# Optimization experiments

Measured on AMD Instinct MI355X. Metric: run time of the kernel, lower is better.

The kernel has to match this reference:

```python
import jax, jax.numpy as jnp
import numpy as np
import math

B, SEQ, H, HKV, D = 2, 2048, 32, 8, 128
BLOCK, LOCAL_BLOCKS, VERT_STRIDE = 64, 16, 8
NB = SEQ // BLOCK


def _build_layout():
    # local + vertical-strided causal block-sparse layout (homo heads),
    # converted from CSR to a padded [NB, max_nnz] column-index table.
    q_idx = np.arange(NB)[:, None]
    k_idx = np.arange(NB)[None, :]
    dense = (k_idx <= q_idx) & ((q_idx - k_idx < LOCAL_BLOCKS) | ((k_idx + 1) % VERT_STRIDE == 0))
    max_nnz = int(dense.sum(1).max())  # == 18 for NB=32, local=16, stride=8
    cols = np.zeros((NB, max_nnz), np.int32)
    valid = np.zeros((NB, max_nnz), np.bool_)
    for i in range(NB):
        c = np.nonzero(dense[i])[0]
        cols[i, :c.size] = c
        valid[i, :c.size] = True
    return jnp.asarray(cols), jnp.asarray(valid)


def setup_inputs() -> dict:
    key = jax.random.key(0)
    kq, kk, kv = jax.random.split(key, 3)
    q = jax.random.normal(kq, (B, SEQ, H, D), jnp.float32)
    k = jax.random.normal(kk, (B, SEQ, HKV, D), jnp.float32)
    v = jax.random.normal(kv, (B, SEQ, HKV, D), jnp.float32)
    layout_cols, layout_mask = _build_layout()
    return {"q": q, "k": k, "v": v, "layout_cols": layout_cols, "layout_mask": layout_mask}


def _attn(q, k, v, layout_cols, layout_mask):
    Bn, S, Hq, Dh = q.shape
    Hkv = k.shape[2]
    g = Hq // Hkv               # GQA group size (q_k_ratio)
    nb, nnz = layout_cols.shape
    blk = S // nb               # block_size
    sm_scale = 1.0 / math.sqrt(Dh)
    # reshape to blocks; keep KV at Hkv heads (no repeat) and group q heads
    qb = q.reshape(Bn, nb, blk, Hkv, g, Dh).transpose(0, 3, 4, 1, 2, 5)  # [B,Hkv,g,nb,blk,D]
    kb = k.reshape(Bn, nb, blk, Hkv, Dh).transpose(0, 3, 1, 2, 4)        # [B,Hkv,nb,blk,D]
    vb = v.reshape(Bn, nb, blk, Hkv, Dh).transpose(0, 3, 1, 2, 4)
    # gather only the attended K/V blocks per query block (honors block sparsity)
    kg = jnp.take(kb, layout_cols, axis=2)  # [B,Hkv,nb,nnz,blk,D]
    vg = jnp.take(vb, layout_cols, axis=2)
    scores = jnp.einsum('bhgqmd,bhqknd->bhgqmkn', qb, kg) * sm_scale  # [B,Hkv,g,nb,blk,nnz,blk]
    # token-level causal mask + padded-column mask (past_len = 0 for prefill)
    q_tok = jnp.arange(nb)[:, None] * blk + jnp.arange(blk)[None, :]            # [nb,blk]
    k_tok = layout_cols[:, :, None] * blk + jnp.arange(blk)[None, None, :]      # [nb,nnz,blk]
    valid = layout_mask[:, None, :, None] & (k_tok[:, None] <= q_tok[:, :, None, None])  # [nb,blk,nnz,blk]
    scores = jnp.where(valid[None, None, None], scores, -jnp.inf)
    p = jax.nn.softmax(scores.reshape(Bn, Hkv, g, nb, blk, nnz * blk), axis=-1).reshape(scores.shape)
    out = jnp.einsum('bhgqmkn,bhqknd->bhgqmd', p, vg)
    return out.transpose(0, 3, 4, 1, 2, 5).reshape(Bn, S, Hq, Dh)


def reference(q, k, v, layout_cols, layout_mask):
    return _attn(q, k, v, layout_cols, layout_mask)
```

## Files before the change

### kernel.cpp

```cpp
#include <hip/hip_runtime.h>

#define B_    2
#define SEQ_  2048
#define H_    32
#define HKV_  8
#define D_    128
#define BLK_  64
#define NB_   32
#define LOCAL_ 16
#define VERT_  8

#define PSTR 72
#define NTASK 512
#define NBLOCK 512

typedef __attribute__((ext_vector_type(8))) short bf16x8;
typedef __attribute__((ext_vector_type(4))) float f32x4;
typedef __attribute__((ext_vector_type(16))) float f32x16;

__device__ __forceinline__ unsigned short f2bf(float f) {
    union { float f; unsigned u; } x; x.f = f;
    unsigned u = x.u;
    return (unsigned short)((u + 0x7FFFu + ((u >> 16) & 1u)) >> 16);
}

__device__ __forceinline__ unsigned pk2(float a, float b) {
#if defined(__has_builtin) && __has_builtin(__builtin_amdgcn_cvt_pk_bf16_f32)
    typedef __attribute__((ext_vector_type(2))) __bf16 bf2;
    bf2 r = __builtin_amdgcn_cvt_pk_bf16_f32(a, b);
    unsigned u; __builtin_memcpy(&u, &r, 4); return u;
#else
    return (unsigned)f2bf(a) | ((unsigned)f2bf(b) << 16);
#endif
}

__device__ __forceinline__ void pswap(unsigned &a, unsigned &b) {
#if defined(__has_builtin) && __has_builtin(__builtin_amdgcn_permlane32_swap)
    auto r = __builtin_amdgcn_permlane32_swap((int)a, (int)b, false, false);
    a = (unsigned)r[0]; b = (unsigned)r[1];
#else
    asm("v_permlane32_swap_b32 %0, %1" : "+v"(a), "+v"(b));
#endif
}

__device__ __forceinline__ f32x16 zero16() {
    f32x16 z;
#pragma unroll
    for (int i = 0; i < 16; ++i) z[i] = 0.f;
    return z;
}

__device__ __forceinline__ int next_valid(int qb, int j) {
    for (++j; j <= qb; ++j)
        if (((qb - j) < LOCAL_) || (((j + 1) & (VERT_ - 1)) == 0)) return j;
    return qb + 1;
}

__device__ __forceinline__ void dma16(const unsigned short* g, unsigned short* l) {
    __builtin_amdgcn_global_load_lds(
        (const __attribute__((address_space(1))) unsigned int*)g,
        (__attribute__((address_space(3))) unsigned int*)l, 16, 0, 0);
}

__global__ __launch_bounds__(256)
void prepass_kernel(const float* __restrict__ kg, const float* __restrict__ vg,
                    unsigned short* __restrict__ Kws, unsigned short* __restrict__ Vws) {
    __shared__ unsigned short Vt[D_ * 72];
    const int bid = blockIdx.x;
    const int b   = bid >> 8;
    const int hkv = (bid >> 5) & 7;
    const int jb  = bid & 31;
    const int tid = threadIdx.x;
    const int rs  = HKV_ * D_;

    const float* kbase = kg + ((size_t)(b * SEQ_ + jb * BLK_) * HKV_ + hkv) * D_;
    const float* vbase = vg + ((size_t)(b * SEQ_ + jb * BLK_) * HKV_ + hkv) * D_;
    unsigned short* Kdst = Kws + ((size_t)(b * 8 + hkv) * SEQ_ + jb * BLK_) * D_;
    unsigned short* Vdst = Vws + ((size_t)(b * 8 + hkv) * NB_ + jb) * (D_ * BLK_);

#pragma unroll
    for (int t = 0; t < 4; ++t) {
        const int q = t * 256 + tid;
        const int row = q >> 4, c = q & 15;
        const float* p = kbase + (size_t)row * rs + c * 8;
        const float4 a = *(const float4*)p;
        const float4 d4 = *(const float4*)(p + 4);
        uint4 u = { pk2(a.x, a.y), pk2(a.z, a.w), pk2(d4.x, d4.y), pk2(d4.z, d4.w) };
        *(uint4*)&Kdst[row * 128 + ((c ^ (row & 15)) << 3)] = u;
    }
#pragma unroll
    for (int t = 0; t < 8; ++t) {
        const int q = t * 256 + tid;
        const int pos = q >> 5, c4 = q & 31;
        const float4 v4 = *(const float4*)(vbase + (size_t)pos * rs + c4 * 4);
        const unsigned u0 = pk2(v4.x, v4.y), u1 = pk2(v4.z, v4.w);
        Vt[(c4 * 4 + 0) * 72 + pos] = (unsigned short)u0;
        Vt[(c4 * 4 + 1) * 72 + pos] = (unsigned short)(u0 >> 16);
        Vt[(c4 * 4 + 2) * 72 + pos] = (unsigned short)u1;
        Vt[(c4 * 4 + 3) * 72 + pos] = (unsigned short)(u1 >> 16);
    }
    __syncthreads();
#pragma unroll
    for (int t = 0; t < 4; ++t) {
        const int q = t * 256 + tid;
        const int d = q >> 3, c = q & 7;
        const uint2 q0 = *(const uint2*)&Vt[d * 72 + c * 8];
        const uint2 q1 = *(const uint2*)&Vt[d * 72 + c * 8 + 4];
        uint4 u = { q0.x, q0.y, q1.x, q1.y };
        *(uint4*)&Vdst[d * 64 + ((c ^ (d & 7)) << 3)] = u;
    }
}

__global__ __launch_bounds__(512, 2)
void sparse_attn_v5(const float* __restrict__ qg, float* __restrict__ outg,
                    const unsigned short* __restrict__ Kws,
                    const unsigned short* __restrict__ Vws,
                    unsigned* __restrict__ ctr) {
    __shared__ __align__(16) unsigned short Kb[2][BLK_ * D_];
    __shared__ __align__(16) unsigned short Vb[2][D_ * BLK_];
    __shared__ unsigned taskLds;

    const int tid  = threadIdx.x;
    const int wave = tid >> 6;
    const int lane = tid & 63;
    const int q5   = lane & 31;
    const int h    = lane >> 5;
    const int hsub = wave >> 1;
    const int rt2  = wave & 1;

    int cskA[8];
#pragma unroll
    for (int dk = 0; dk < 8; ++dk) cskA[dk] = ((((dk * 2) | h) ^ (lane & 15)) << 3);
    int csvB[4];
#pragma unroll
    for (int kc = 0; kc < 4; ++kc) csvB[kc] = ((((kc * 2) | h) ^ (lane & 7)) << 3);

    const float c2 = 0.12751649736230723f;
    const short oneb = (short)0x3F80;
    const bf16x8 ones = {oneb, oneb, oneb, oneb, oneb, oneb, oneb, oneb};

    for (;;) {
        __syncthreads();
        if (tid == 0) taskLds = atomicAdd(ctr, 1u);
        __syncthreads();
        const unsigned t = taskLds;
        if (t >= NTASK) break;

        const int qb  = 31 - (int)(t >> 4);
        const int bh  = (int)(t & 15);
        const int b   = bh >> 3;
        const int hkv = bh & 7;
        const int head = hkv * 4 + hsub;

        const unsigned short* Kbh = Kws + (size_t)(b * 8 + hkv) * SEQ_ * D_;
        const unsigned short* Vbh = Vws + (size_t)(b * 8 + hkv) * NB_ * (D_ * BLK_);

        int j = next_valid(qb, -1);
        {
            const size_t off = (size_t)j * (BLK_ * D_);
#pragma unroll
            for (int i = 0; i < 2; ++i) {
                dma16(Kbh + off + i * 4096 + tid * 8, &Kb[0][i * 4096 + wave * 512]);
                dma16(Vbh + off + i * 4096 + tid * 8, &Vb[0][i * 4096 + wave * 512]);
            }
        }

        bf16x8 qf[8];
        {
            const int row = qb * BLK_ + rt2 * 32 + q5;
            const float* qp = qg + ((size_t)(b * SEQ_ + row) * H_ + head) * D_ + h * 8;
#pragma unroll
            for (int dk = 0; dk < 8; ++dk) {
                const float4 a = *(const float4*)(qp + dk * 16);
                const float4 c = *(const float4*)(qp + dk * 16 + 4);
                uint4 u = { pk2(a.x, a.y), pk2(a.z, a.w), pk2(c.x, c.y), pk2(c.z, c.w) };
                __builtin_memcpy(&qf[dk], &u, 16);
            }
        }

        f32x16 lacc = zero16();
        f32x16 o_acc[4];
#pragma unroll
        for (int dt = 0; dt < 4; ++dt) o_acc[dt] = zero16();

        __syncthreads();
        int it = 0;
        while (j <= qb) {
            const int jn = next_valid(qb, j);
            const int cur = it & 1;
            if (jn <= qb) {
                const size_t off = (size_t)jn * (BLK_ * D_);
#pragma unroll
                for (int i = 0; i < 2; ++i) {
                    dma16(Kbh + off + i * 4096 + tid * 8, &Kb[cur ^ 1][i * 4096 + wave * 512]);
                    dma16(Vbh + off + i * 4096 + tid * 8, &Vb[cur ^ 1][i * 4096 + wave * 512]);
                }
            }

            const bool diag  = (j == qb);
            const bool diagw = diag && (rt2 == 0);

            const unsigned short* kb = Kb[cur];
            f32x16 s0 = zero16(), s1 = zero16();
            {
                const unsigned short* k0r = kb + q5 * 128;
                const unsigned short* k1r = kb + (32 + q5) * 128;
#pragma unroll
                for (int dk = 0; dk < 8; ++dk) {
                    const bf16x8 kf0 = *(const bf16x8*)(k0r + cskA[dk]);
                    s0 = __builtin_amdgcn_mfma_f32_32x32x16_bf16(kf0, qf[dk], s0, 0, 0, 0);
                }
                if (!diagw) {
#pragma unroll
                    for (int dk = 0; dk < 8; ++dk) {
                        const bf16x8 kf1 = *(const bf16x8*)(k1r + cskA[dk]);
                        s1 = __builtin_amdgcn_mfma_f32_32x32x16_bf16(kf1, qf[dk], s1, 0, 0, 0);
                    }
                }
            }

            if (diag) {
                if (rt2 == 0) {
#pragma unroll
                    for (int r = 0; r < 16; ++r) {
                        const int crow = (r & 3) + 8 * (r >> 2) + 4 * h;
                        if (crow > q5) s0[r] = -INFINITY;
                    }
                } else {
#pragma unroll
                    for (int r = 0; r < 16; ++r) {
                        const int crow = (r & 3) + 8 * (r >> 2) + 4 * h;
                        if (crow > q5) s1[r] = -INFINITY;
                    }
                }
            }

#pragma unroll
            for (int r = 0; r < 16; ++r) s0[r] = exp2f(s0[r] * c2);
            if (!diagw) {
#pragma unroll
                for (int r = 0; r < 16; ++r) s1[r] = exp2f(s1[r] * c2);
            }

            bf16x8 pa[4];
#pragma unroll
            for (int kc = 0; kc < 4; ++kc) {
                if (kc >= 2 && diagw) continue;
                const f32x16 &pp = (kc >= 2) ? s1 : s0;
                const int b0 = (kc & 1) * 8;
                unsigned A0 = pk2(pp[b0 + 0], pp[b0 + 1]);
                unsigned B0 = pk2(pp[b0 + 4], pp[b0 + 5]);
                unsigned A1 = pk2(pp[b0 + 2], pp[b0 + 3]);
                unsigned B1 = pk2(pp[b0 + 6], pp[b0 + 7]);
                pswap(A0, B0);
                pswap(A1, B1);
                uint4 u = { A0, A1, B0, B1 };
                __builtin_memcpy(&pa[kc], &u, 16);
                lacc = __builtin_amdgcn_mfma_f32_32x32x16_bf16(pa[kc], ones, lacc, 0, 0, 0);
            }

            const unsigned short* vb = Vb[cur];
#pragma unroll
            for (int dt = 0; dt < 4; ++dt) {
                const unsigned short* vrow = vb + (dt * 32 + q5) * 64;
#pragma unroll
                for (int kc = 0; kc < 4; ++kc) {
                    if (kc >= 2 && diagw) continue;
                    const bf16x8 vf = *(const bf16x8*)(vrow + csvB[kc]);
                    o_acc[dt] = __builtin_amdgcn_mfma_f32_32x32x16_bf16(pa[kc], vf, o_acc[dt], 0, 0, 0);
                }
            }

            __syncthreads();
            j = jn; ++it;
        }

        const int rowbase = qb * BLK_ + rt2 * 32;
#pragma unroll
        for (int r = 0; r < 16; ++r) {
            const int row = rowbase + (r & 3) + 8 * (r >> 2) + 4 * h;
            const float inv = 1.0f / lacc[r];
            float* op = outg + ((size_t)(b * SEQ_ + row) * H_ + head) * D_ + q5;
            op[0]  = o_acc[0][r] * inv;
            op[32] = o_acc[1][r] * inv;
            op[64] = o_acc[2][r] * inv;
            op[96] = o_acc[3][r] * inv;
        }
    }
}

#define KSTR 136
#define VSTR 72
__global__ __launch_bounds__(1024)
void sparse_attn_v1(const float* __restrict__ qg, const float* __restrict__ kg,
                    const float* __restrict__ vg, float* __restrict__ outg,
                    unsigned* __restrict__ ctr) {
    __shared__ __align__(16) unsigned short Klds[BLK_ * KSTR];
    __shared__ __align__(16) unsigned short Vlds[D_ * VSTR];
    __shared__ __align__(16) unsigned short Plds[16 * 16 * PSTR];
    __shared__ unsigned taskLds;

    const int tid  = threadIdx.x;
    const int wave = tid >> 6;
    const int lane = tid & 63;
    const int l15  = lane & 15;
    const int quad = lane >> 4;
    const int hsub = wave >> 2;
    const int rt   = wave & 3;

    const int srow0 = tid >> 5, srow1 = srow0 + 32;
    const int sc4   = tid & 31;
    const int kld0  = srow0 * KSTR + sc4 * 4, kld1 = srow1 * KSTR + sc4 * 4;
    const int vd    = sc4 * 4;
    const int vskew = (sc4 & 7) << 3;
    const int vp0   = (srow0 + vskew) & 63, vp1 = (srow1 + vskew) & 63;
    const size_t stoff0 = (size_t)srow0 * (HKV_ * D_) + sc4 * 4;
    const size_t stoff1 = (size_t)srow1 * (HKV_ * D_) + sc4 * 4;

    const float c2 = 0.12751649736230723f;
    const short oneb = (short)0x3F80;
    const bf16x8 ones = {oneb, oneb, oneb, oneb, oneb, oneb, oneb, oneb};
    unsigned short* pl = &Plds[wave * 16 * PSTR];

    for (;;) {
        __syncthreads();
        if (tid == 0) taskLds = atomicAdd(ctr, 1u);
        __syncthreads();
        const unsigned t = taskLds;
        if (t >= NTASK) break;
        const int qb  = 31 - (int)(t >> 4);
        const int bh  = (int)(t & 15);
        const int b   = bh >> 3;
        const int hkv = bh & 7;
        const int head = hkv * 4 + hsub;
        const float* kbase = kg + ((size_t)(b * SEQ_) * HKV_ + hkv) * D_;
        const float* vbase = vg + ((size_t)(b * SEQ_) * HKV_ + hkv) * D_;
        bf16x8 qf[4];
        {
            const int row = qb * BLK_ + rt * 16 + l15;
            const float* qp = qg + ((size_t)(b * SEQ_ + row) * H_ + head) * D_;
#pragma unroll
            for (int s = 0; s < 4; ++s) {
                const float4 a = *(const float4*)(qp + s * 32 + quad * 8);
                const float4 c = *(const float4*)(qp + s * 32 + quad * 8 + 4);
                uint4 u = { pk2(a.x, a.y), pk2(a.z, a.w), pk2(c.x, c.y), pk2(c.z, c.w) };
                __builtin_memcpy(&qf[s], &u, 16);
            }
        }
        f32x4 lacc = f32x4{0.f, 0.f, 0.f, 0.f};
        f32x4 o_acc[8];
#pragma unroll
        for (int t8 = 0; t8 < 8; ++t8) o_acc[t8] = f32x4{0.f, 0.f, 0.f, 0.f};
        int j = next_valid(qb, -1);
        float4 kpr0, kpr1, vpr0, vpr1;
        {
            const float* kp = kbase + (size_t)j * BLK_ * HKV_ * D_;
            const float* vp = vbase + (size_t)j * BLK_ * HKV_ * D_;
            kpr0 = *(const float4*)(kp + stoff0); kpr1 = *(const float4*)(kp + stoff1);
            vpr0 = *(const float4*)(vp + stoff0); vpr1 = *(const float4*)(vp + stoff1);
        }
        while (j <= qb) {
            const int jn = next_valid(qb, j);
            __syncthreads();
            {
                uint2 u0 = { pk2(kpr0.x, kpr0.y), pk2(kpr0.z, kpr0.w) };
                uint2 u1 = { pk2(kpr1.x, kpr1.y), pk2(kpr1.z, kpr1.w) };
                *(uint2*)&Klds[kld0] = u0;
                *(uint2*)&Klds[kld1] = u1;
                unsigned a0 = pk2(vpr0.x, vpr0.y), a1 = pk2(vpr0.z, vpr0.w);
                Vlds[(vd + 0) * VSTR + vp0] = (unsigned short)a0;
                Vlds[(vd + 1) * VSTR + vp0] = (unsigned short)(a0 >> 16);
                Vlds[(vd + 2) * VSTR + vp0] = (unsigned short)a1;
                Vlds[(vd + 3) * VSTR + vp0] = (unsigned short)(a1 >> 16);
                unsigned b0 = pk2(vpr1.x, vpr1.y), b1 = pk2(vpr1.z, vpr1.w);
                Vlds[(vd + 0) * VSTR + vp1] = (unsigned short)b0;
                Vlds[(vd + 1) * VSTR + vp1] = (unsigned short)(b0 >> 16);
                Vlds[(vd + 2) * VSTR + vp1] = (unsigned short)b1;
                Vlds[(vd + 3) * VSTR + vp1] = (unsigned short)(b1 >> 16);
            }
            __syncthreads();
            if (jn <= qb) {
                const float* kp = kbase + (size_t)jn * BLK_ * HKV_ * D_;
                const float* vp = vbase + (size_t)jn * BLK_ * HKV_ * D_;
                kpr0 = *(const float4*)(kp + stoff0); kpr1 = *(const float4*)(kp + stoff1);
                vpr0 = *(const float4*)(vp + stoff0); vpr1 = *(const float4*)(vp + stoff1);
            }
            f32x4 sacc[4];
#pragma unroll
            for (int t4 = 0; t4 < 4; ++t4) {
                f32x4 acc = f32x4{0.f, 0.f, 0.f, 0.f};
#pragma unroll
                for (int s = 0; s < 4; ++s) {
                    const bf16x8 kf = *(const bf16x8*)&Klds[(t4 * 16 + l15) * KSTR + s * 32 + quad * 8];
                    acc = __builtin_amdgcn_mfma_f32_16x16x32_bf16(qf[s], kf, acc, 0, 0, 0);
                }
                sacc[t4] = acc;
            }
            if (j == qb) {
                const int rowbase = rt * 16 + quad * 4;
#pragma unroll
                for (int t4 = 0; t4 < 4; ++t4) {
                    const int col = t4 * 16 + l15;
#pragma unroll
                    for (int r = 0; r < 4; ++r)
                        if (col > rowbase + r) sacc[t4][r] = -INFINITY;
                }
            }
#pragma unroll
            for (int t4 = 0; t4 < 4; ++t4) {
                const float p0 = exp2f(sacc[t4][0] * c2);
                const float p1 = exp2f(sacc[t4][1] * c2);
                const float p2 = exp2f(sacc[t4][2] * c2);
                const float p3 = exp2f(sacc[t4][3] * c2);
                const unsigned u01 = pk2(p0, p1), u23 = pk2(p2, p3);
                const int cb = t4 * 16 + l15;
                pl[(quad * 4 + 0) * PSTR + cb] = (unsigned short)u01;
                pl[(quad * 4 + 1) * PSTR + cb] = (unsigned short)(u01 >> 16);
                pl[(quad * 4 + 2) * PSTR + cb] = (unsigned short)u23;
                pl[(quad * 4 + 3) * PSTR + cb] = (unsigned short)(u23 >> 16);
            }
#pragma unroll
            for (int s2 = 0; s2 < 2; ++s2) {
                const bf16x8 pf = *(const bf16x8*)&pl[l15 * PSTR + s2 * 32 + quad * 8];
                lacc = __builtin_amdgcn_mfma_f32_16x16x32_bf16(pf, ones, lacc, 0, 0, 0);
                const int k0 = s2 * 32 + quad * 8;
#pragma unroll
                for (int t8 = 0; t8 < 8; ++t8) {
                    const int n  = t8 * 16 + l15;
                    const int p2 = (k0 + (((n >> 2) & 7) << 3)) & 63;
                    const bf16x8 vf = *(const bf16x8*)&Vlds[n * VSTR + p2];
                    o_acc[t8] = __builtin_amdgcn_mfma_f32_16x16x32_bf16(pf, vf, o_acc[t8], 0, 0, 0);
                }
            }
            j = jn;
        }
        const int orow = qb * BLK_ + rt * 16 + quad * 4;
#pragma unroll
        for (int r = 0; r < 4; ++r) {
            const float inv_l = 1.0f / lacc[r];
            float* op = outg + ((size_t)(b * SEQ_ + orow + r) * H_ + head) * D_;
#pragma unroll
            for (int t8 = 0; t8 < 8; ++t8)
                op[t8 * 16 + l15] = o_acc[t8][r] * inv_l;
        }
    }
}

extern "C" void kernel_launch(void* const* d_in, const int* in_sizes, int n_in,
                              void* d_out, int out_size, void* d_ws, size_t ws_size,
                              hipStream_t stream) {
    const float* q = (const float*)d_in[0];
    const float* k = (const float*)d_in[1];
    const float* v = (const float*)d_in[2];
    float* out = (float*)d_out;

    const size_t kws_elems = (size_t)B_ * HKV_ * SEQ_ * D_;
    const size_t need = 256 + 2 * kws_elems * sizeof(unsigned short);
    if (ws_size >= need) {
        unsigned short* Kws = (unsigned short*)((char*)d_ws + 256);
        unsigned short* Vws = Kws + kws_elems;
        hipMemsetAsync(d_ws, 0, 256, stream);
        prepass_kernel<<<dim3(B_ * HKV_ * NB_), dim3(256), 0, stream>>>(k, v, Kws, Vws);
        sparse_attn_v5<<<dim3(NBLOCK), dim3(512), 0, stream>>>(q, out, Kws, Vws, (unsigned*)d_ws);
    } else {
        hipMemsetAsync(d_ws, 0, sizeof(unsigned), stream);
        sparse_attn_v1<<<dim3(NBLOCK), dim3(1024), 0, stream>>>(q, k, v, out, (unsigned*)d_ws);
    }
}
```

Before: 240.5 us.

## Split attention per batch with paired-query-block KV sharing and static grids

Replaces the persistent atomic-counter task loop with statically indexed grids, so the counter memset goes away. Batch 1 runs in a 1024-thread kernel where each block handles two adjacent query blocks and loads the union of their KV blocks once; waves skip KV blocks their own query block does not attend. Batch 0 runs in a separate 512-thread kernel with one query block per workgroup. The intent is to cut atomic and memset overhead and reuse KV tiles across query blocks. In exchange, the two batch launches run back to back, the static order loses the largest-first load balancing, and each launch exposes less parallelism.

```diff
diff --git a/kernel.cpp b/kernel.cpp
--- a/kernel.cpp
+++ b/kernel.cpp
@@ -12,7 +12,6 @@
 
 #define PSTR 72
 #define NTASK 512
-#define NBLOCK 512
 
 typedef __attribute__((ext_vector_type(8))) short bf16x8;
 typedef __attribute__((ext_vector_type(4))) float f32x4;
@@ -50,10 +49,16 @@
     return z;
 }
 
+__device__ __forceinline__ bool vfor(int q, int j) {
+    return (j <= q) && (((q - j) < LOCAL_) || (((j + 1) & (VERT_ - 1)) == 0));
+}
 __device__ __forceinline__ int next_valid(int qb, int j) {
-    for (++j; j <= qb; ++j)
-        if (((qb - j) < LOCAL_) || (((j + 1) & (VERT_ - 1)) == 0)) return j;
+    for (++j; j <= qb; ++j) if (vfor(qb, j)) return j;
     return qb + 1;
+}
+__device__ __forceinline__ int next_valid2(int hi, int j) {
+    for (++j; j <= hi; ++j) if (vfor(hi, j) || vfor(hi - 1, j)) return j;
+    return hi + 1;
 }
 
 __device__ __forceinline__ void dma16(const unsigned short* g, unsigned short* l) {
@@ -112,13 +117,12 @@
 }
 
 __global__ __launch_bounds__(512, 2)
-void sparse_attn_v5(const float* __restrict__ qg, float* __restrict__ outg,
-                    const unsigned short* __restrict__ Kws,
-                    const unsigned short* __restrict__ Vws,
-                    unsigned* __restrict__ ctr) {
+void sparse_attn_v7s(const float* __restrict__ qg, float* __restrict__ outg,
+                     const unsigned short* __restrict__ Kws,
+                     const unsigned short* __restrict__ Vws,
+                     int bsel) {
     __shared__ __align__(16) unsigned short Kb[2][BLK_ * D_];
     __shared__ __align__(16) unsigned short Vb[2][D_ * BLK_];
-    __shared__ unsigned taskLds;
 
     const int tid  = threadIdx.x;
     const int wave = tid >> 6;
@@ -139,65 +143,225 @@
     const short oneb = (short)0x3F80;
     const bf16x8 ones = {oneb, oneb, oneb, oneb, oneb, oneb, oneb, oneb};
 
-    for (;;) {
+    const int bid = blockIdx.x;
+    const int hkv = bid & 7;
+    const int qb  = bid >> 3;
+    const int b   = bsel;
+    const int head = hkv * 4 + hsub;
+
+    const unsigned short* Kbh = Kws + (size_t)(b * 8 + hkv) * SEQ_ * D_;
+    const unsigned short* Vbh = Vws + (size_t)(b * 8 + hkv) * NB_ * (D_ * BLK_);
+
+    int j = next_valid(qb, -1);
+    {
+        const size_t off = (size_t)j * (BLK_ * D_);
+#pragma unroll
+        for (int i = 0; i < 2; ++i) {
+            dma16(Kbh + off + i * 4096 + tid * 8, &Kb[0][i * 4096 + wave * 512]);
+            dma16(Vbh + off + i * 4096 + tid * 8, &Vb[0][i * 4096 + wave * 512]);
+        }
+    }
+
+    bf16x8 qf[8];
+    {
+        const int row = qb * BLK_ + rt2 * 32 + q5;
+        const float* qp = qg + ((size_t)(b * SEQ_ + row) * H_ + head) * D_ + h * 8;
+#pragma unroll
+        for (int dk = 0; dk < 8; ++dk) {
+            const float4 a = *(const float4*)(qp + dk * 16);
+            const float4 c = *(const float4*)(qp + dk * 16 + 4);
+            uint4 u = { pk2(a.x, a.y), pk2(a.z, a.w), pk2(c.x, c.y), pk2(c.z, c.w) };
+            __builtin_memcpy(&qf[dk], &u, 16);
+        }
+    }
+
+    f32x16 lacc = zero16();
+    f32x16 o_acc[4];
+#pragma unroll
+    for (int dt = 0; dt < 4; ++dt) o_acc[dt] = zero16();
+
+    __syncthreads();
+    int it = 0;
+    while (j <= qb) {
+        const int jn = next_valid(qb, j);
+        const int cur = it & 1;
+        if (jn <= qb) {
+            const size_t off = (size_t)jn * (BLK_ * D_);
+#pragma unroll
+            for (int i = 0; i < 2; ++i) {
+                dma16(Kbh + off + i * 4096 + tid * 8, &Kb[cur ^ 1][i * 4096 + wave * 512]);
+                dma16(Vbh + off + i * 4096 + tid * 8, &Vb[cur ^ 1][i * 4096 + wave * 512]);
+            }
+        }
+
+        const bool diag  = (j == qb);
+        const bool diagw = diag && (rt2 == 0);
+
+        const unsigned short* kb = Kb[cur];
+        f32x16 s0 = zero16(), s1 = zero16();
+        {
+            const unsigned short* k0r = kb + q5 * 128;
+            const unsigned short* k1r = kb + (32 + q5) * 128;
+#pragma unroll
+            for (int dk = 0; dk < 8; ++dk) {
+                const bf16x8 kf0 = *(const bf16x8*)(k0r + cskA[dk]);
+                s0 = __builtin_amdgcn_mfma_f32_32x32x16_bf16(kf0, qf[dk], s0, 0, 0, 0);
+            }
+            if (!diagw) {
+#pragma unroll
+                for (int dk = 0; dk < 8; ++dk) {
+                    const bf16x8 kf1 = *(const bf16x8*)(k1r + cskA[dk]);
+                    s1 = __builtin_amdgcn_mfma_f32_32x32x16_bf16(kf1, qf[dk], s1, 0, 0, 0);
+                }
+            }
+        }
+
+        if (diag) {
+            if (rt2 == 0) {
+#pragma unroll
+                for (int r = 0; r < 16; ++r) {
+                    const int crow = (r & 3) + 8 * (r >> 2) + 4 * h;
+                    if (crow > q5) s0[r] = -INFINITY;
+                }
+            } else {
+#pragma unroll
+                for (int r = 0; r < 16; ++r) {
+                    const int crow = (r & 3) + 8 * (r >> 2) + 4 * h;
+                    if (crow > q5) s1[r] = -INFINITY;
+                }
+            }
+        }
+
+#pragma unroll
+        for (int r = 0; r < 16; ++r) s0[r] = exp2f(s0[r] * c2);
+        if (!diagw) {
+#pragma unroll
+            for (int r = 0; r < 16; ++r) s1[r] = exp2f(s1[r] * c2);
+        }
+
+        bf16x8 pa[4];
+#pragma unroll
+        for (int kc = 0; kc < 4; ++kc) {
+            if (kc >= 2 && diagw) continue;
+            const f32x16 &pp = (kc >= 2) ? s1 : s0;
+            const int b0 = (kc & 1) * 8;
+            unsigned A0 = pk2(pp[b0 + 0], pp[b0 + 1]);
+            unsigned B0 = pk2(pp[b0 + 4], pp[b0 + 5]);
+            unsigned A1 = pk2(pp[b0 + 2], pp[b0 + 3]);
+            unsigned B1 = pk2(pp[b0 + 6], pp[b0 + 7]);
+            pswap(A0, B0);
+            pswap(A1, B1);
+            uint4 u = { A0, A1, B0, B1 };
+            __builtin_memcpy(&pa[kc], &u, 16);
+            lacc = __builtin_amdgcn_mfma_f32_32x32x16_bf16(pa[kc], ones, lacc, 0, 0, 0);
+        }
+
+        const unsigned short* vb = Vb[cur];
+#pragma unroll
+        for (int dt = 0; dt < 4; ++dt) {
+            const unsigned short* vrow = vb + (dt * 32 + q5) * 64;
+#pragma unroll
+            for (int kc = 0; kc < 4; ++kc) {
+                if (kc >= 2 && diagw) continue;
+                const bf16x8 vf = *(const bf16x8*)(vrow + csvB[kc]);
+                o_acc[dt] = __builtin_amdgcn_mfma_f32_32x32x16_bf16(pa[kc], vf, o_acc[dt], 0, 0, 0);
+            }
+        }
+
         __syncthreads();
-        if (tid == 0) taskLds = atomicAdd(ctr, 1u);
-        __syncthreads();
-        const unsigned t = taskLds;
-        if (t >= NTASK) break;
-
-        const int qb  = 31 - (int)(t >> 4);
-        const int bh  = (int)(t & 15);
-        const int b   = bh >> 3;
-        const int hkv = bh & 7;
-        const int head = hkv * 4 + hsub;
-
-        const unsigned short* Kbh = Kws + (size_t)(b * 8 + hkv) * SEQ_ * D_;
-        const unsigned short* Vbh = Vws + (size_t)(b * 8 + hkv) * NB_ * (D_ * BLK_);
-
-        int j = next_valid(qb, -1);
-        {
-            const size_t off = (size_t)j * (BLK_ * D_);
-#pragma unroll
-            for (int i = 0; i < 2; ++i) {
-                dma16(Kbh + off + i * 4096 + tid * 8, &Kb[0][i * 4096 + wave * 512]);
-                dma16(Vbh + off + i * 4096 + tid * 8, &Vb[0][i * 4096 + wave * 512]);
-            }
-        }
-
-        bf16x8 qf[8];
-        {
-            const int row = qb * BLK_ + rt2 * 32 + q5;
-            const float* qp = qg + ((size_t)(b * SEQ_ + row) * H_ + head) * D_ + h * 8;
-#pragma unroll
-            for (int dk = 0; dk < 8; ++dk) {
-                const float4 a = *(const float4*)(qp + dk * 16);
-                const float4 c = *(const float4*)(qp + dk * 16 + 4);
-                uint4 u = { pk2(a.x, a.y), pk2(a.z, a.w), pk2(c.x, c.y), pk2(c.z, c.w) };
-                __builtin_memcpy(&qf[dk], &u, 16);
-            }
-        }
-
-        f32x16 lacc = zero16();
-        f32x16 o_acc[4];
-#pragma unroll
-        for (int dt = 0; dt < 4; ++dt) o_acc[dt] = zero16();
-
-        __syncthreads();
-        int it = 0;
-        while (j <= qb) {
-            const int jn = next_valid(qb, j);
-            const int cur = it & 1;
-            if (jn <= qb) {
-                const size_t off = (size_t)jn * (BLK_ * D_);
-#pragma unroll
-                for (int i = 0; i < 2; ++i) {
-                    dma16(Kbh + off + i * 4096 + tid * 8, &Kb[cur ^ 1][i * 4096 + wave * 512]);
-                    dma16(Vbh + off + i * 4096 + tid * 8, &Vb[cur ^ 1][i * 4096 + wave * 512]);
-                }
-            }
-
-            const bool diag  = (j == qb);
+        j = jn; ++it;
+    }
+
+    const int rowbase = qb * BLK_ + rt2 * 32;
+#pragma unroll
+    for (int r = 0; r < 16; ++r) {
+        const int row = rowbase + (r & 3) + 8 * (r >> 2) + 4 * h;
+        const float inv = 1.0f / lacc[r];
+        float* op = outg + ((size_t)(b * SEQ_ + row) * H_ + head) * D_ + q5;
+        op[0]  = o_acc[0][r] * inv;
+        op[32] = o_acc[1][r] * inv;
+        op[64] = o_acc[2][r] * inv;
+        op[96] = o_acc[3][r] * inv;
+    }
+}
+
+__global__ __launch_bounds__(1024)
+void sparse_attn_v7p(const float* __restrict__ qg, float* __restrict__ outg,
+                     const unsigned short* __restrict__ Kws,
+                     const unsigned short* __restrict__ Vws,
+                     int bsel) {
+    __shared__ __align__(16) unsigned short Kb[2][BLK_ * D_];
+    __shared__ __align__(16) unsigned short Vb[2][D_ * BLK_];
+
+    const int tid  = threadIdx.x;
+    const int wave = tid >> 6;
+    const int lane = tid & 63;
+    const int q5   = lane & 31;
+    const int h    = lane >> 5;
+    const int hsub = wave >> 2;
+    const int rt4  = wave & 3;
+
+    int cskA[8];
+#pragma unroll
+    for (int dk = 0; dk < 8; ++dk) cskA[dk] = ((((dk * 2) | h) ^ (lane & 15)) << 3);
+    int csvB[4];
+#pragma unroll
+    for (int kc = 0; kc < 4; ++kc) csvB[kc] = ((((kc * 2) | h) ^ (lane & 7)) << 3);
+
+    const float c2 = 0.12751649736230723f;
+    const short oneb = (short)0x3F80;
+    const bf16x8 ones = {oneb, oneb, oneb, oneb, oneb, oneb, oneb, oneb};
+
+    const int bid = blockIdx.x;
+    const int hkv = bid & 7;
+    const int qbp = bid >> 3;
+    const int hi  = qbp * 2 + 1;
+    const int qb_w = qbp * 2 + (rt4 >> 1);
+    const int rt2 = rt4 & 1;
+    const int b   = bsel;
+    const int head = hkv * 4 + hsub;
+
+    const unsigned short* Kbh = Kws + (size_t)(b * 8 + hkv) * SEQ_ * D_;
+    const unsigned short* Vbh = Vws + (size_t)(b * 8 + hkv) * NB_ * (D_ * BLK_);
+
+    int j = next_valid2(hi, -1);
+    {
+        const size_t off = (size_t)j * (BLK_ * D_);
+        dma16(Kbh + off + tid * 8, &Kb[0][wave * 512]);
+        dma16(Vbh + off + tid * 8, &Vb[0][wave * 512]);
+    }
+
+    bf16x8 qf[8];
+    {
+        const int row = qbp * 128 + rt4 * 32 + q5;
+        const float* qp = qg + ((size_t)(b * SEQ_ + row) * H_ + head) * D_ + h * 8;
+#pragma unroll
+        for (int dk = 0; dk < 8; ++dk) {
+            const float4 a = *(const float4*)(qp + dk * 16);
+            const float4 c = *(const float4*)(qp + dk * 16 + 4);
+            uint4 u = { pk2(a.x, a.y), pk2(a.z, a.w), pk2(c.x, c.y), pk2(c.z, c.w) };
+            __builtin_memcpy(&qf[dk], &u, 16);
+        }
+    }
+
+    f32x16 lacc = zero16();
+    f32x16 o_acc[4];
+#pragma unroll
+    for (int dt = 0; dt < 4; ++dt) o_acc[dt] = zero16();
+
+    __syncthreads();
+    int it = 0;
+    while (j <= hi) {
+        const int jn = next_valid2(hi, j);
+        const int cur = it & 1;
+        if (jn <= hi) {
+            const size_t off = (size_t)jn * (BLK_ * D_);
+            dma16(Kbh + off + tid * 8, &Kb[cur ^ 1][wave * 512]);
+            dma16(Vbh + off + tid * 8, &Vb[cur ^ 1][wave * 512]);
+        }
+
+        if (vfor(qb_w, j)) {
+            const bool diag  = (j == qb_w);
             const bool diagw = diag && (rt2 == 0);
 
             const unsigned short* kb = Kb[cur];
@@ -270,22 +434,22 @@
                     o_acc[dt] = __builtin_amdgcn_mfma_f32_32x32x16_bf16(pa[kc], vf, o_acc[dt], 0, 0, 0);
                 }
             }
-
-            __syncthreads();
-            j = jn; ++it;
-        }
-
-        const int rowbase = qb * BLK_ + rt2 * 32;
-#pragma unroll
-        for (int r = 0; r < 16; ++r) {
-            const int row = rowbase + (r & 3) + 8 * (r >> 2) + 4 * h;
-            const float inv = 1.0f / lacc[r];
-            float* op = outg + ((size_t)(b * SEQ_ + row) * H_ + head) * D_ + q5;
-            op[0]  = o_acc[0][r] * inv;
-            op[32] = o_acc[1][r] * inv;
-            op[64] = o_acc[2][r] * inv;
-            op[96] = o_acc[3][r] * inv;
-        }
+        }
+
+        __syncthreads();
+        j = jn; ++it;
+    }
+
+    const int rowbase = qbp * 128 + rt4 * 32;
+#pragma unroll
+    for (int r = 0; r < 16; ++r) {
+        const int row = rowbase + (r & 3) + 8 * (r >> 2) + 4 * h;
+        const float inv = 1.0f / lacc[r];
+        float* op = outg + ((size_t)(b * SEQ_ + row) * H_ + head) * D_ + q5;
+        op[0]  = o_acc[0][r] * inv;
+        op[32] = o_acc[1][r] * inv;
+        op[64] = o_acc[2][r] * inv;
+        op[96] = o_acc[3][r] * inv;
     }
 }
 
@@ -459,11 +623,11 @@
     if (ws_size >= need) {
         unsigned short* Kws = (unsigned short*)((char*)d_ws + 256);
         unsigned short* Vws = Kws + kws_elems;
-        hipMemsetAsync(d_ws, 0, 256, stream);
         prepass_kernel<<<dim3(B_ * HKV_ * NB_), dim3(256), 0, stream>>>(k, v, Kws, Vws);
-        sparse_attn_v5<<<dim3(NBLOCK), dim3(512), 0, stream>>>(q, out, Kws, Vws, (unsigned*)d_ws);
+        sparse_attn_v7p<<<dim3(128), dim3(1024), 0, stream>>>(q, out, Kws, Vws, 1);
+        sparse_attn_v7s<<<dim3(256), dim3(512), 0, stream>>>(q, out, Kws, Vws, 0);
     } else {
         hipMemsetAsync(d_ws, 0, sizeof(unsigned), stream);
-        sparse_attn_v1<<<dim3(NBLOCK), dim3(1024), 0, stream>>>(q, k, v, out, (unsigned*)d_ws);
-    }
-}
+        sparse_attn_v1<<<dim3(256), dim3(1024), 0, stream>>>(q, k, v, out, (unsigned*)d_ws);
+    }
+}
```

After: 713.8 us. 197% more time.

## Split QK/PV into per-half passes and compute row sums with lane reductions

Applied to the files above, without the earlier changes.

The attention loop now processes each 32-key half in turn: scores, exp, packing and the PV MFMAs run per half, so only one score accumulator is live instead of two. The row-sum MFMA against a ones vector is replaced by a per-lane scalar sum of the bf16-rounded probabilities, combined across lane halves with a permlane swap and redistributed with ds_bpermute in the epilogue. Precomputed swizzle offsets are dropped, and launch bounds move from 2 to 4 blocks per SM to push register usage down for higher occupancy. The tradeoffs are possible spills under the tighter register cap and extra VALU and permute work for the sums. The fallback kernel's grid is also halved.

```diff
diff --git a/kernel.cpp b/kernel.cpp
--- a/kernel.cpp
+++ b/kernel.cpp
@@ -41,6 +41,13 @@
 #else
     asm("v_permlane32_swap_b32 %0, %1" : "+v"(a), "+v"(b));
 #endif
+}
+
+__device__ __forceinline__ float bflo(unsigned u) {
+    unsigned v = u << 16; float f; __builtin_memcpy(&f, &v, 4); return f;
+}
+__device__ __forceinline__ float bfhi(unsigned u) {
+    unsigned v = u & 0xFFFF0000u; float f; __builtin_memcpy(&f, &v, 4); return f;
 }
 
 __device__ __forceinline__ f32x16 zero16() {
@@ -111,8 +118,8 @@
     }
 }
 
-__global__ __launch_bounds__(512, 2)
-void sparse_attn_v5(const float* __restrict__ qg, float* __restrict__ outg,
+__global__ __launch_bounds__(512, 4)
+void sparse_attn_v8(const float* __restrict__ qg, float* __restrict__ outg,
                     const unsigned short* __restrict__ Kws,
                     const unsigned short* __restrict__ Vws,
                     unsigned* __restrict__ ctr) {
@@ -125,19 +132,12 @@
     const int lane = tid & 63;
     const int q5   = lane & 31;
     const int h    = lane >> 5;
+    const int l15  = lane & 15;
+    const int l7   = lane & 7;
     const int hsub = wave >> 1;
     const int rt2  = wave & 1;
 
-    int cskA[8];
-#pragma unroll
-    for (int dk = 0; dk < 8; ++dk) cskA[dk] = ((((dk * 2) | h) ^ (lane & 15)) << 3);
-    int csvB[4];
-#pragma unroll
-    for (int kc = 0; kc < 4; ++kc) csvB[kc] = ((((kc * 2) | h) ^ (lane & 7)) << 3);
-
     const float c2 = 0.12751649736230723f;
-    const short oneb = (short)0x3F80;
-    const bf16x8 ones = {oneb, oneb, oneb, oneb, oneb, oneb, oneb, oneb};
 
     for (;;) {
         __syncthreads();
@@ -178,7 +178,7 @@
             }
         }
 
-        f32x16 lacc = zero16();
+        float llane = 0.f;
         f32x16 o_acc[4];
 #pragma unroll
         for (int dt = 0; dt < 4; ++dt) o_acc[dt] = zero16();
@@ -199,87 +199,75 @@
 
             const bool diag  = (j == qb);
             const bool diagw = diag && (rt2 == 0);
-
             const unsigned short* kb = Kb[cur];
-            f32x16 s0 = zero16(), s1 = zero16();
-            {
-                const unsigned short* k0r = kb + q5 * 128;
-                const unsigned short* k1r = kb + (32 + q5) * 128;
+            const unsigned short* vb = Vb[cur];
+
+            auto HALF = [&](int kh, bool maskit) {
+                const unsigned short* krow = kb + (kh * 32 + q5) * 128;
+                f32x16 s = zero16();
 #pragma unroll
                 for (int dk = 0; dk < 8; ++dk) {
-                    const bf16x8 kf0 = *(const bf16x8*)(k0r + cskA[dk]);
-                    s0 = __builtin_amdgcn_mfma_f32_32x32x16_bf16(kf0, qf[dk], s0, 0, 0, 0);
-                }
-                if (!diagw) {
-#pragma unroll
-                    for (int dk = 0; dk < 8; ++dk) {
-                        const bf16x8 kf1 = *(const bf16x8*)(k1r + cskA[dk]);
-                        s1 = __builtin_amdgcn_mfma_f32_32x32x16_bf16(kf1, qf[dk], s1, 0, 0, 0);
-                    }
-                }
-            }
-
-            if (diag) {
-                if (rt2 == 0) {
+                    const int ck = ((((dk * 2) | h) ^ l15) << 3);
+                    const bf16x8 kf = *(const bf16x8*)(krow + ck);
+                    s = __builtin_amdgcn_mfma_f32_32x32x16_bf16(kf, qf[dk], s, 0, 0, 0);
+                }
+                if (maskit) {
 #pragma unroll
                     for (int r = 0; r < 16; ++r) {
                         const int crow = (r & 3) + 8 * (r >> 2) + 4 * h;
-                        if (crow > q5) s0[r] = -INFINITY;
+                        if (crow > q5) s[r] = -INFINITY;
                     }
-                } else {
-#pragma unroll
-                    for (int r = 0; r < 16; ++r) {
-                        const int crow = (r & 3) + 8 * (r >> 2) + 4 * h;
-                        if (crow > q5) s1[r] = -INFINITY;
+                }
+#pragma unroll
+                for (int r = 0; r < 16; ++r) s[r] = exp2f(s[r] * c2);
+
+#pragma unroll
+                for (int kq = 0; kq < 2; ++kq) {
+                    const int b0 = kq * 8;
+                    unsigned A0 = pk2(s[b0 + 0], s[b0 + 1]);
+                    unsigned B0 = pk2(s[b0 + 4], s[b0 + 5]);
+                    unsigned A1 = pk2(s[b0 + 2], s[b0 + 3]);
+                    unsigned B1 = pk2(s[b0 + 6], s[b0 + 7]);
+                    llane += ((bflo(A0) + bfhi(A0)) + (bflo(B0) + bfhi(B0)))
+                           + ((bflo(A1) + bfhi(A1)) + (bflo(B1) + bfhi(B1)));
+                    pswap(A0, B0);
+                    pswap(A1, B1);
+                    bf16x8 pa;
+                    uint4 u = { A0, A1, B0, B1 };
+                    __builtin_memcpy(&pa, &u, 16);
+                    const int kc = kh * 2 + kq;
+                    const int cv = ((((kc * 2) | h) ^ l7) << 3);
+#pragma unroll
+                    for (int dt = 0; dt < 4; ++dt) {
+                        const bf16x8 vf = *(const bf16x8*)(vb + (dt * 32 + q5) * 64 + cv);
+                        o_acc[dt] = __builtin_amdgcn_mfma_f32_32x32x16_bf16(pa, vf, o_acc[dt], 0, 0, 0);
                     }
                 }
-            }
-
-#pragma unroll
-            for (int r = 0; r < 16; ++r) s0[r] = exp2f(s0[r] * c2);
-            if (!diagw) {
-#pragma unroll
-                for (int r = 0; r < 16; ++r) s1[r] = exp2f(s1[r] * c2);
-            }
-
-            bf16x8 pa[4];
-#pragma unroll
-            for (int kc = 0; kc < 4; ++kc) {
-                if (kc >= 2 && diagw) continue;
-                const f32x16 &pp = (kc >= 2) ? s1 : s0;
-                const int b0 = (kc & 1) * 8;
-                unsigned A0 = pk2(pp[b0 + 0], pp[b0 + 1]);
-                unsigned B0 = pk2(pp[b0 + 4], pp[b0 + 5]);
-                unsigned A1 = pk2(pp[b0 + 2], pp[b0 + 3]);
-                unsigned B1 = pk2(pp[b0 + 6], pp[b0 + 7]);
-                pswap(A0, B0);
-                pswap(A1, B1);
-                uint4 u = { A0, A1, B0, B1 };
-                __builtin_memcpy(&pa[kc], &u, 16);
-                lacc = __builtin_amdgcn_mfma_f32_32x32x16_bf16(pa[kc], ones, lacc, 0, 0, 0);
-            }
-
-            const unsigned short* vb = Vb[cur];
-#pragma unroll
-            for (int dt = 0; dt < 4; ++dt) {
-                const unsigned short* vrow = vb + (dt * 32 + q5) * 64;
-#pragma unroll
-                for (int kc = 0; kc < 4; ++kc) {
-                    if (kc >= 2 && diagw) continue;
-                    const bf16x8 vf = *(const bf16x8*)(vrow + csvB[kc]);
-                    o_acc[dt] = __builtin_amdgcn_mfma_f32_32x32x16_bf16(pa[kc], vf, o_acc[dt], 0, 0, 0);
-                }
-            }
+            };
+
+            HALF(0, diag && (rt2 == 0));
+            if (!diagw) HALF(1, diag && (rt2 == 1));
 
             __syncthreads();
             j = jn; ++it;
         }
 
+        unsigned lu; __builtin_memcpy(&lu, &llane, 4);
+        unsigned la = lu, lb = lu;
+        pswap(la, lb);
+        float fa, fb; __builtin_memcpy(&fa, &la, 4); __builtin_memcpy(&fb, &lb, 4);
+        const float l_q5 = fa + fb;
+        int lfull_i; __builtin_memcpy(&lfull_i, &l_q5, 4);
+
         const int rowbase = qb * BLK_ + rt2 * 32;
 #pragma unroll
         for (int r = 0; r < 16; ++r) {
-            const int row = rowbase + (r & 3) + 8 * (r >> 2) + 4 * h;
-            const float inv = 1.0f / lacc[r];
+            const int cb  = (r & 3) + 8 * (r >> 2);
+            const int crow = cb + 4 * h;
+            const int li = __builtin_amdgcn_ds_bpermute(crow << 2, lfull_i);
+            float lr; __builtin_memcpy(&lr, &li, 4);
+            const float inv = 1.0f / lr;
+            const int row = rowbase + crow;
             float* op = outg + ((size_t)(b * SEQ_ + row) * H_ + head) * D_ + q5;
             op[0]  = o_acc[0][r] * inv;
             op[32] = o_acc[1][r] * inv;
@@ -461,9 +449,9 @@
         unsigned short* Vws = Kws + kws_elems;
         hipMemsetAsync(d_ws, 0, 256, stream);
         prepass_kernel<<<dim3(B_ * HKV_ * NB_), dim3(256), 0, stream>>>(k, v, Kws, Vws);
-        sparse_attn_v5<<<dim3(NBLOCK), dim3(512), 0, stream>>>(q, out, Kws, Vws, (unsigned*)d_ws);
+        sparse_attn_v8<<<dim3(NBLOCK), dim3(512), 0, stream>>>(q, out, Kws, Vws, (unsigned*)d_ws);
     } else {
         hipMemsetAsync(d_ws, 0, sizeof(unsigned), stream);
-        sparse_attn_v1<<<dim3(NBLOCK), dim3(1024), 0, stream>>>(q, k, v, out, (unsigned*)d_ws);
-    }
-}
+        sparse_attn_v1<<<dim3(256), dim3(1024), 0, stream>>>(q, k, v, out, (unsigned*)d_ws);
+    }
+}
```

New measurement: 300.4 us. +24.9%, slower.
